# Kernel tuning notes

Hardware: AMD Instinct MI355X
Metric: run time of the kernel (lower is better)

## Reference

```python
import jax, jax.numpy as jnp
import numpy as np

B, C, H, W, K = 16, 1, 768, 768, 512


def setup_inputs() -> dict:
    key = jax.random.key(0)
    k1, k2, k3 = jax.random.split(key, 3)
    pre_denses = jax.random.normal(k1, (B, C, H, W), dtype=jnp.float32)
    gt_denses = jax.random.normal(k2, (B, C, H, W), dtype=jnp.float32)
    gt_cors = jax.random.randint(k3, (B, K, 2), 0, min(H, W), dtype=jnp.int32)
    return {"pre_denses": pre_denses, "gt_denses": gt_denses, "gt_cors": gt_cors}


def _peak_mask(pre):
    # The original pads by 2, shift-compares, then crops by 1; this is equivalent
    # to a zero-pad-by-1 4-neighbor local-max test at every original pixel.
    p = jnp.pad(pre, ((0, 0), (0, 0), (1, 1), (1, 1)))
    left = p[:, :, 1:-1, 2:]
    right = p[:, :, 1:-1, :-2]
    up = p[:, :, 2:, 1:-1]
    down = p[:, :, :-2, 1:-1]
    return (pre > left) & (pre > right) & (pre > up) & (pre > down)


def reference(pre_denses, gt_denses, gt_cors):
    b, c, h, w = pre_denses.shape
    # --- loss1: peak-position loss ---
    pre_mask = _peak_mask(pre_denses)  # [B,1,H,W] bool
    batch_idx = jnp.arange(b)[:, None]           # [B,1]
    ys = gt_cors[:, :, 1]                        # row index
    xs = gt_cors[:, :, 0]                        # col index
    gt_mask = jnp.zeros((b, c, h, w), dtype=bool).at[batch_idx, 0, ys, xs].set(True)
    mask1 = jnp.bitwise_xor(pre_mask, gt_mask).astype(jnp.float32)  # C_head = 1
    error = (pre_denses - gt_denses) ** 2
    l1 = jnp.mean(jnp.sum(mask1 * error, axis=(1, 2, 3)))
    # --- loss2: weighted MSE ---
    head = (gt_denses > 0).astype(jnp.float32)
    mse_mask = 5.0 * head + (1.0 - head)  # C_head=5, C_no_head=1
    l2 = jnp.mean(jnp.sum(mse_mask * error, axis=(1, 2, 3)))
    return l1 + l2
```

## Files before the change

### kernel.cpp

```cpp
#include <hip/hip_runtime.h>

#define BDIM 16
#define HDIM 768
#define WDIM 768
#define KCOR 512
constexpr int HW = HDIM * WDIM;
constexpr int TOTAL = BDIM * HW;
constexpr int TOTALQ = TOTAL / 4;

__global__ __launch_bounds__(256) void main_kernel(
    const float* __restrict__ pre,
    const float* __restrict__ gt,
    float* __restrict__ out) {

    float acc = 0.0f;
    const int nthreads = gridDim.x * blockDim.x;
    for (int q = blockIdx.x * blockDim.x + threadIdx.x; q < TOTALQ; q += nthreads) {
        const int idx = q * 4;
        const int rem = idx % HW;
        const int row = rem / WDIM;
        const int x   = rem % WDIM;

        const float4 c4 = *(const float4*)(pre + idx);
        const float4 g4 = *(const float4*)(gt + idx);
        const float  lft = (x > 0)          ? pre[idx - 1] : 0.0f;
        const float  rgt = (x + 4 < WDIM)   ? pre[idx + 4] : 0.0f;
        const float4 u4 = (row > 0)         ? *(const float4*)(pre + idx - WDIM)
                                            : make_float4(0.f, 0.f, 0.f, 0.f);
        const float4 d4 = (row < HDIM - 1)  ? *(const float4*)(pre + idx + WDIM)
                                            : make_float4(0.f, 0.f, 0.f, 0.f);

        const float c[4]  = {c4.x, c4.y, c4.z, c4.w};
        const float g[4]  = {g4.x, g4.y, g4.z, g4.w};
        const float u[4]  = {u4.x, u4.y, u4.z, u4.w};
        const float d[4]  = {d4.x, d4.y, d4.z, d4.w};
        const float lr[6] = {lft, c[0], c[1], c[2], c[3], rgt};

        #pragma unroll
        for (int j = 0; j < 4; ++j) {
            const bool peak = (c[j] > lr[j]) && (c[j] > lr[j + 2]) &&
                              (c[j] > u[j]) && (c[j] > d[j]);
            float e = c[j] - g[j];
            e *= e;
            const float wt = (g[j] > 0.0f ? 5.0f : 1.0f) + (peak ? 1.0f : 0.0f);
            acc += wt * e;
        }
    }

    #pragma unroll
    for (int off = 32; off > 0; off >>= 1) acc += __shfl_down(acc, off);

    __shared__ float lds[4];
    const int wave = threadIdx.x >> 6;
    const int lane = threadIdx.x & 63;
    if (lane == 0) lds[wave] = acc;
    __syncthreads();
    if (threadIdx.x == 0) {
        const float s = lds[0] + lds[1] + lds[2] + lds[3];
        atomicAdd(out, s * (1.0f / (float)BDIM));
    }
}

__global__ __launch_bounds__(KCOR) void corr_kernel(
    const float* __restrict__ pre,
    const float* __restrict__ gt,
    const int* __restrict__ cors,
    float* __restrict__ out) {

    __shared__ int scoord[KCOR];
    const int b = blockIdx.x;
    const int k = threadIdx.x;
    const int x = cors[(b * KCOR + k) * 2 + 0];
    const int y = cors[(b * KCOR + k) * 2 + 1];
    const int packed = y * WDIM + x;
    scoord[k] = packed;
    __syncthreads();

    bool dup = false;
    for (int k2 = 0; k2 < k; ++k2) dup |= (scoord[k2] == packed);

    float contrib = 0.0f;
    if (!dup) {
        const int idx = b * HW + packed;
        const float c = pre[idx];
        const float l = (x > 0)        ? pre[idx - 1]    : 0.0f;
        const float r = (x < WDIM - 1) ? pre[idx + 1]    : 0.0f;
        const float u = (y > 0)        ? pre[idx - WDIM] : 0.0f;
        const float d = (y < HDIM - 1) ? pre[idx + WDIM] : 0.0f;
        const bool peak = (c > l) && (c > r) && (c > u) && (c > d);
        float e = c - gt[idx];
        e *= e;
        contrib = (peak ? -1.0f : 1.0f) * e;
    }

    #pragma unroll
    for (int off = 32; off > 0; off >>= 1) contrib += __shfl_down(contrib, off);

    __shared__ float lds[8];
    const int wave = threadIdx.x >> 6;
    const int lane = threadIdx.x & 63;
    if (lane == 0) lds[wave] = contrib;
    __syncthreads();
    if (threadIdx.x == 0) {
        float s = 0.0f;
        #pragma unroll
        for (int i = 0; i < 8; ++i) s += lds[i];
        atomicAdd(out, s * (1.0f / (float)BDIM));
    }
}

extern "C" void kernel_launch(void* const* d_in, const int* in_sizes, int n_in,
                              void* d_out, int out_size, void* d_ws, size_t ws_size,
                              hipStream_t stream) {
    const float* pre  = (const float*)d_in[0];
    const float* gt   = (const float*)d_in[1];
    const int*   cors = (const int*)d_in[2];

    float* out = (float*)d_out;

    hipMemsetAsync(out, 0, sizeof(float), stream);

    main_kernel<<<1024, 256, 0, stream>>>(pre, gt, out);

    corr_kernel<<<BDIM, KCOR, 0, stream>>>(pre, gt, cors, out);
}
```

Before: 122.1 us.

## Fuse correction pass into main kernel and replace atomics with two-stage reduction

Merges the coordinate-correction work into the first 16 blocks of the main stencil kernel. Replaces the grid-stride loop with one 8-element tile per thread over a full grid of blocks, and makes neighbor loads unconditional through clamped offsets. Per-block partials go to workspace and a single-block kernel reduces them, which removes the memset and the atomics. The aim is fewer launches and better memory-level parallelism. The cost is a much larger grid, and the 16 correction blocks do serial duplicate checks in LDS that may delay the tail.

Result: no change. 123.3 us (+1.0%).

```diff
diff --git a/kernel.cpp b/kernel.cpp
--- a/kernel.cpp
+++ b/kernel.cpp
@@ -6,38 +6,93 @@
 #define KCOR 512
 constexpr int HW = HDIM * WDIM;
 constexpr int TOTAL = BDIM * HW;
-constexpr int TOTALQ = TOTAL / 4;
+constexpr int NTHREADS_TOT = TOTAL / 8;
+constexpr int BLOCK = 256;
+constexpr int NBLK = NTHREADS_TOT / BLOCK;
 
-__global__ __launch_bounds__(256) void main_kernel(
+__global__ __launch_bounds__(BLOCK) void fused_kernel(
     const float* __restrict__ pre,
     const float* __restrict__ gt,
-    float* __restrict__ out) {
+    const int* __restrict__ cors,
+    float* __restrict__ ws_partials) {
+
+    __shared__ int scoord[KCOR];
+    __shared__ float lred[BLOCK / 64];
 
     float acc = 0.0f;
-    const int nthreads = gridDim.x * blockDim.x;
-    for (int q = blockIdx.x * blockDim.x + threadIdx.x; q < TOTALQ; q += nthreads) {
-        const int idx = q * 4;
+
+    if (blockIdx.x < BDIM) {
+        const int b = blockIdx.x;
+        for (int k = threadIdx.x; k < KCOR; k += BLOCK) {
+            const int x = cors[(b * KCOR + k) * 2 + 0];
+            const int y = cors[(b * KCOR + k) * 2 + 1];
+            scoord[k] = y * WDIM + x;
+        }
+        __syncthreads();
+        for (int k = threadIdx.x; k < KCOR; k += BLOCK) {
+            const int packed = scoord[k];
+            bool dup = false;
+            for (int k2 = 0; k2 < k; ++k2) dup |= (scoord[k2] == packed);
+            if (!dup) {
+                const int y = packed / WDIM;
+                const int x = packed - y * WDIM;
+                const int idx = b * HW + packed;
+                const float c = pre[idx];
+                const float l = (x > 0)        ? pre[idx - 1]    : 0.0f;
+                const float r = (x < WDIM - 1) ? pre[idx + 1]    : 0.0f;
+                const float u = (y > 0)        ? pre[idx - WDIM] : 0.0f;
+                const float d = (y < HDIM - 1) ? pre[idx + WDIM] : 0.0f;
+                const bool peak = (c > l) && (c > r) && (c > u) && (c > d);
+                float e = c - gt[idx];
+                e *= e;
+                acc += (peak ? -1.0f : 1.0f) * e;
+            }
+        }
+        __syncthreads();
+    }
+
+    {
+        const int t   = blockIdx.x * BLOCK + threadIdx.x;
+        const int idx = t * 8;
         const int rem = idx % HW;
         const int row = rem / WDIM;
         const int x   = rem % WDIM;
 
-        const float4 c4 = *(const float4*)(pre + idx);
-        const float4 g4 = *(const float4*)(gt + idx);
-        const float  lft = (x > 0)          ? pre[idx - 1] : 0.0f;
-        const float  rgt = (x + 4 < WDIM)   ? pre[idx + 4] : 0.0f;
-        const float4 u4 = (row > 0)         ? *(const float4*)(pre + idx - WDIM)
-                                            : make_float4(0.f, 0.f, 0.f, 0.f);
-        const float4 d4 = (row < HDIM - 1)  ? *(const float4*)(pre + idx + WDIM)
-                                            : make_float4(0.f, 0.f, 0.f, 0.f);
+        const int uoff = (row > 0)         ? WDIM : 0;
+        const int doff = (row < HDIM - 1)  ? WDIM : 0;
+        const int loff = (x > 0)           ? 1 : 0;
+        const int roff = (x + 8 < WDIM)    ? 8 : 0;
 
-        const float c[4]  = {c4.x, c4.y, c4.z, c4.w};
-        const float g[4]  = {g4.x, g4.y, g4.z, g4.w};
-        const float u[4]  = {u4.x, u4.y, u4.z, u4.w};
-        const float d[4]  = {d4.x, d4.y, d4.z, d4.w};
-        const float lr[6] = {lft, c[0], c[1], c[2], c[3], rgt};
+        const float4 c0 = *(const float4*)(pre + idx);
+        const float4 c1 = *(const float4*)(pre + idx + 4);
+        const float4 g0 = *(const float4*)(gt  + idx);
+        const float4 g1 = *(const float4*)(gt  + idx + 4);
+        const float4 ua = *(const float4*)(pre + idx - uoff);
+        const float4 ub = *(const float4*)(pre + idx + 4 - uoff);
+        const float4 da = *(const float4*)(pre + idx + doff);
+        const float4 db = *(const float4*)(pre + idx + 4 + doff);
+        const float  lraw = pre[idx - loff];
+        const float  rraw = pre[idx + roff];
+
+        const bool hasu = (uoff != 0), hasd = (doff != 0);
+        const float lft = (loff != 0) ? lraw : 0.0f;
+        const float rgt = (roff != 0) ? rraw : 0.0f;
+
+        const float c[8] = {c0.x, c0.y, c0.z, c0.w, c1.x, c1.y, c1.z, c1.w};
+        const float g[8] = {g0.x, g0.y, g0.z, g0.w, g1.x, g1.y, g1.z, g1.w};
+        const float u[8] = {hasu ? ua.x : 0.f, hasu ? ua.y : 0.f,
+                            hasu ? ua.z : 0.f, hasu ? ua.w : 0.f,
+                            hasu ? ub.x : 0.f, hasu ? ub.y : 0.f,
+                            hasu ? ub.z : 0.f, hasu ? ub.w : 0.f};
+        const float d[8] = {hasd ? da.x : 0.f, hasd ? da.y : 0.f,
+                            hasd ? da.z : 0.f, hasd ? da.w : 0.f,
+                            hasd ? db.x : 0.f, hasd ? db.y : 0.f,
+                            hasd ? db.z : 0.f, hasd ? db.w : 0.f};
+        const float lr[10] = {lft, c[0], c[1], c[2], c[3],
+                              c[4], c[5], c[6], c[7], rgt};
 
         #pragma unroll
-        for (int j = 0; j < 4; ++j) {
+        for (int j = 0; j < 8; ++j) {
             const bool peak = (c[j] > lr[j]) && (c[j] > lr[j + 2]) &&
                               (c[j] > u[j]) && (c[j] > d[j]);
             float e = c[j] - g[j];
@@ -49,63 +104,35 @@
 
     #pragma unroll
     for (int off = 32; off > 0; off >>= 1) acc += __shfl_down(acc, off);
-
-    __shared__ float lds[4];
     const int wave = threadIdx.x >> 6;
     const int lane = threadIdx.x & 63;
-    if (lane == 0) lds[wave] = acc;
-    __syncthreads();
-    if (threadIdx.x == 0) {
-        const float s = lds[0] + lds[1] + lds[2] + lds[3];
-        atomicAdd(out, s * (1.0f / (float)BDIM));
-    }
-}
-
-__global__ __launch_bounds__(KCOR) void corr_kernel(
-    const float* __restrict__ pre,
-    const float* __restrict__ gt,
-    const int* __restrict__ cors,
-    float* __restrict__ out) {
-
-    __shared__ int scoord[KCOR];
-    const int b = blockIdx.x;
-    const int k = threadIdx.x;
-    const int x = cors[(b * KCOR + k) * 2 + 0];
-    const int y = cors[(b * KCOR + k) * 2 + 1];
-    const int packed = y * WDIM + x;
-    scoord[k] = packed;
-    __syncthreads();
-
-    bool dup = false;
-    for (int k2 = 0; k2 < k; ++k2) dup |= (scoord[k2] == packed);
-
-    float contrib = 0.0f;
-    if (!dup) {
-        const int idx = b * HW + packed;
-        const float c = pre[idx];
-        const float l = (x > 0)        ? pre[idx - 1]    : 0.0f;
-        const float r = (x < WDIM - 1) ? pre[idx + 1]    : 0.0f;
-        const float u = (y > 0)        ? pre[idx - WDIM] : 0.0f;
-        const float d = (y < HDIM - 1) ? pre[idx + WDIM] : 0.0f;
-        const bool peak = (c > l) && (c > r) && (c > u) && (c > d);
-        float e = c - gt[idx];
-        e *= e;
-        contrib = (peak ? -1.0f : 1.0f) * e;
-    }
-
-    #pragma unroll
-    for (int off = 32; off > 0; off >>= 1) contrib += __shfl_down(contrib, off);
-
-    __shared__ float lds[8];
-    const int wave = threadIdx.x >> 6;
-    const int lane = threadIdx.x & 63;
-    if (lane == 0) lds[wave] = contrib;
+    if (lane == 0) lred[wave] = acc;
     __syncthreads();
     if (threadIdx.x == 0) {
         float s = 0.0f;
         #pragma unroll
-        for (int i = 0; i < 8; ++i) s += lds[i];
-        atomicAdd(out, s * (1.0f / (float)BDIM));
+        for (int i = 0; i < BLOCK / 64; ++i) s += lred[i];
+        ws_partials[blockIdx.x] = s;
+    }
+}
+
+__global__ __launch_bounds__(BLOCK) void reduce_kernel(
+    const float* __restrict__ ws_partials,
+    float* __restrict__ out) {
+    float acc = 0.0f;
+    for (int i = threadIdx.x; i < NBLK; i += BLOCK) acc += ws_partials[i];
+    #pragma unroll
+    for (int off = 32; off > 0; off >>= 1) acc += __shfl_down(acc, off);
+    __shared__ float lred[BLOCK / 64];
+    const int wave = threadIdx.x >> 6;
+    const int lane = threadIdx.x & 63;
+    if (lane == 0) lred[wave] = acc;
+    __syncthreads();
+    if (threadIdx.x == 0) {
+        float s = 0.0f;
+        #pragma unroll
+        for (int i = 0; i < BLOCK / 64; ++i) s += lred[i];
+        out[0] = s * (1.0f / (float)BDIM);
     }
 }
 
@@ -115,12 +142,9 @@
     const float* pre  = (const float*)d_in[0];
     const float* gt   = (const float*)d_in[1];
     const int*   cors = (const int*)d_in[2];
+    float* out = (float*)d_out;
+    float* partials = (float*)d_ws;
 
-    float* out = (float*)d_out;
-
-    hipMemsetAsync(out, 0, sizeof(float), stream);
-
-    main_kernel<<<1024, 256, 0, stream>>>(pre, gt, out);
-
-    corr_kernel<<<BDIM, KCOR, 0, stream>>>(pre, gt, cors, out);
+    fused_kernel<<<NBLK, BLOCK, 0, stream>>>(pre, gt, cors, partials);
+    reduce_kernel<<<1, BLOCK, 0, stream>>>(partials, out);
 }
```
